# Kernel optimization log

Hardware: AMD Instinct MI355X
Metric: run time of the kernel (lower is better)

## Reference

```python
import jax, jax.numpy as jnp
import numpy as np

N = 100000   # nodes
E = 1250000  # directed edges
F = 32       # node_features
H = 64       # hidden_channels
C = 10       # num_classes
NEG_SLOPE = 0.2  # GATConv default LeakyReLU slope


def _glorot(key, shape):
    fan_in = shape[0]
    return jax.random.normal(key, shape, jnp.float32) / np.sqrt(fan_in)


def setup_inputs() -> dict:
    k = jax.random.split(jax.random.key(0), 16)
    x = jax.random.normal(k[0], (N, F), jnp.float32)
    edge_index = jax.random.randint(k[1], (2, E), 0, N, dtype=jnp.int32)
    return {
        "x": x,
        "edge_index": edge_index,
        # GCNConv 1
        "W1": _glorot(k[2], (F, H)), "b1": jnp.zeros((H,), jnp.float32),
        # GATConv (heads=1)
        "W2": _glorot(k[3], (H, H)),
        "a_src": _glorot(k[4], (H,)), "a_dst": _glorot(k[5], (H,)),
        "b2": jnp.zeros((H,), jnp.float32),
        # GCNConv 3
        "W3": _glorot(k[6], (H, H)), "b3": jnp.zeros((H,), jnp.float32),
        # optimization head
        "Wopt": _glorot(k[7], (H, C)), "bopt": jnp.zeros((C,), jnp.float32),
        # bottleneck detector MLP
        "Wb1": _glorot(k[8], (H, 32)), "bb1": jnp.zeros((32,), jnp.float32),
        "Wb2": _glorot(k[9], (32, 1)), "bb2": jnp.zeros((1,), jnp.float32),
    }


def _gcn_conv(x, W, b, src, dst, n):
    # PyG GCNConv: self-loops already appended to src/dst by caller.
    h = x @ W  # [n, out]
    deg = jnp.zeros((n,), x.dtype).at[dst].add(1.0)
    dinv = jax.lax.rsqrt(jnp.maximum(deg, 1e-12))
    norm = dinv[src] * dinv[dst]  # [e]
    msg = h[src] * norm[:, None]  # gather + scale
    out = jnp.zeros_like(h).at[dst].add(msg)  # scatter-add
    return out + b


def _gat_conv(x, W, a_src, a_dst, b, src, dst, n):
    # PyG GATConv, heads=1: self-loops already appended.
    h = x @ W  # [n, out]
    alpha_s = h @ a_src  # [n]
    alpha_d = h @ a_dst  # [n]
    e = jax.nn.leaky_relu(alpha_s[src] + alpha_d[dst], NEG_SLOPE)  # [e]
    # softmax over incoming edges of each dst node
    emax = jax.ops.segment_max(e, dst, num_segments=n)
    p = jnp.exp(e - emax[dst])
    denom = jax.ops.segment_sum(p, dst, num_segments=n)
    alpha = p / denom[dst]
    out = jnp.zeros_like(h).at[dst].add(h[src] * alpha[:, None])
    return out + b


def reference(x, edge_index, W1, b1, W2, a_src, a_dst, b2, W3, b3,
              Wopt, bopt, Wb1, bb1, Wb2, bb2):
    n = x.shape[0]
    loops = jnp.arange(n, dtype=edge_index.dtype)
    src = jnp.concatenate([edge_index[0], loops])
    dst = jnp.concatenate([edge_index[1], loops])

    h = jax.nn.relu(_gcn_conv(x, W1, b1, src, dst, n))
    h = jax.nn.relu(_gat_conv(h, W2, a_src, a_dst, b2, src, dst, n))
    h = jax.nn.relu(_gcn_conv(h, W3, b3, src, dst, n))

    optimizations = h @ Wopt + bopt                     # [n, C]
    bottlenecks = jax.nn.sigmoid(jax.nn.relu(h @ Wb1 + bb1) @ Wb2 + bb2)  # [n, 1]
    graph_embedding = h.mean(axis=0)                    # [H]
    return optimizations, bottlenecks, graph_embedding
```

## Files before the change

### kernel.cpp

```cpp
#include <hip/hip_runtime.h>
#include <hip/hip_bf16.h>


#define CAP 64
#define NP2 128
#define NB2MAX 800

__device__ __forceinline__ int uwave(){
  return __builtin_amdgcn_readfirstlane(threadIdx.x >> 6);
}
__device__ __forceinline__ unsigned short f2bf(float f){
  unsigned u = __float_as_uint(f);
  return (unsigned short)((u + 0x7fffu + ((u >> 16) & 1u)) >> 16);
}
__device__ __forceinline__ float bfl(unsigned u){ return __uint_as_float(u << 16); }
__device__ __forceinline__ float bfh(unsigned u){ return __uint_as_float(u & 0xffff0000u); }
__device__ __forceinline__ float rdlane(float v, int l){
  return __uint_as_float(__builtin_amdgcn_readlane(__float_as_uint(v), l));
}

__global__ void k_setup(const float* __restrict__ Wopt, const float* __restrict__ bopt,
                        const float* __restrict__ Wb1, const float* __restrict__ bb1,
                        float* __restrict__ Wcat, float* __restrict__ bcat,
                        int* __restrict__ bcnt, int* __restrict__ ghist,
                        unsigned short* __restrict__ tb,
                        unsigned short* __restrict__ xh, float* __restrict__ emb_acc,
                        float* __restrict__ als, int n, int nb2){
  int i = blockIdx.x*blockDim.x + threadIdx.x;
  if (i < nb2) bcnt[i] = 0;
  int tid = threadIdx.x;
  if (blockIdx.x == 1 && tid < 65) ghist[tid] = 0;
  if (blockIdx.x == 0){
    for (int j = tid; j < 4096; j += 256){
      int f = j >> 6, c = j & 63;
      float w = 0.f;
      if (c < 10)       w = Wopt[f*10 + c];
      else if (c >= 32) w = Wb1[f*32 + (c-32)];
      Wcat[j] = w;
    }
    if (tid < 64){
      float b = 0.f;
      if (tid < 10)       b = bopt[tid];
      else if (tid >= 32) b = bb1[tid-32];
      bcat[tid] = b;
      tb[(size_t)n*64 + tid] = 0;
      emb_acc[tid] = 0.f;
      if (tid == 0) als[n] = 0.f;
    }
    if (tid >= 64 && tid < 96) xh[(size_t)n*32 + (tid-64)] = 0;
  }
}

__global__ __launch_bounds__(256) void k_part(const int* __restrict__ src,
                        const int* __restrict__ dst,
                        uint2* __restrict__ pairs, int* __restrict__ bcnt,
                        int e, int nb2, int pbcap){
  __shared__ int lcnt[NB2MAX];
  __shared__ int lbase[NB2MAX];
  int tid = threadIdx.x;
  for (int j = tid; j < nb2; j += 256) lcnt[j] = 0;
  __syncthreads();
  int i0 = blockIdx.x*2048 + tid*8;
  int d[8], s[8], bk[8], lp[8];
  int nv = e - i0;
  if (nv > 8) nv = 8;
  if (nv < 0) nv = 0;
  if (nv == 8){
    int4 d0 = *(const int4*)(dst + i0), d1 = *(const int4*)(dst + i0 + 4);
    int4 s0 = *(const int4*)(src + i0), s1 = *(const int4*)(src + i0 + 4);
    d[0]=d0.x; d[1]=d0.y; d[2]=d0.z; d[3]=d0.w;
    d[4]=d1.x; d[5]=d1.y; d[6]=d1.z; d[7]=d1.w;
    s[0]=s0.x; s[1]=s0.y; s[2]=s0.z; s[3]=s0.w;
    s[4]=s1.x; s[5]=s1.y; s[6]=s1.z; s[7]=s1.w;
  } else {
    #pragma unroll
    for (int j = 0; j < 8; j++){ d[j] = 0; s[j] = 0; }
    for (int j = 0; j < nv; j++){ d[j] = dst[i0+j]; s[j] = src[i0+j]; }
  }
  #pragma unroll
  for (int j = 0; j < 8; j++){
    if (j < nv){
      bk[j] = d[j] >> 7;
      lp[j] = atomicAdd(&lcnt[bk[j]], 1);
    }
  }
  __syncthreads();
  for (int j = tid; j < nb2; j += 256){
    int c = lcnt[j];
    if (c) lbase[j] = atomicAdd(&bcnt[j], c);
  }
  __syncthreads();
  #pragma unroll
  for (int j = 0; j < 8; j++){
    if (j < nv){
      int p = lbase[bk[j]] + lp[j];
      if (p < pbcap)
        pairs[(size_t)bk[j]*pbcap + p] = make_uint2((unsigned)d[j], (unsigned)s[j]);
    }
  }
}

__global__ __launch_bounds__(256) void k_fill(const uint2* __restrict__ pairs,
                        const int* __restrict__ bcnt, int* __restrict__ cnt,
                        int* __restrict__ adj, int* __restrict__ ghist,
                        const float* __restrict__ x, unsigned short* __restrict__ xh,
                        int pbcap, int n){
  __shared__ int lc[NP2];
  __shared__ int ladj[NP2*CAP];
  __shared__ int lh[65];
  int b = blockIdx.x;
  int lo = b << 7;
  int nn = min(NP2, n - lo);
  int tid = threadIdx.x;
  for (int j = tid; j < NP2; j += 256) lc[j] = 0;
  if (tid < 65) lh[tid] = 0;
  int4 nfill = make_int4(n, n, n, n);
  for (int j = tid; j < NP2*CAP/4; j += 256) ((int4*)ladj)[j] = nfill;
  __syncthreads();
  int m = bcnt[b];
  if (m > pbcap) m = pbcap;
  const uint2* pb = pairs + (size_t)b*pbcap;
  for (int j = tid; j < m; j += 256){
    uint2 p = pb[j];
    int r = (int)p.x - lo;
    int pos = atomicAdd(&lc[r], 1);
    if (pos < CAP) ladj[(r << 6) + pos] = (int)p.y;
  }
  __syncthreads();
  if (tid < nn){
    int c = lc[tid];
    cnt[lo + tid] = c;
    atomicAdd(&lh[min(c, CAP)], 1);
  }
  __syncthreads();
  if (tid < 65 && lh[tid]) atomicAdd(&ghist[tid], lh[tid]);
  int tot = nn << 4;
  uint4* ga = (uint4*)(adj + (size_t)lo*CAP);
  const uint4* la = (const uint4*)ladj;
  for (int j = tid; j < tot; j += 256) ga[j] = la[j];
  int tf = nn << 3;
  const float4* xr4 = (const float4*)(x + (size_t)lo*32);
  uint2* xo = (uint2*)(xh + (size_t)lo*32);
  for (int j = tid; j < tf; j += 256){
    int r = j >> 3;
    float dv = rsqrtf((float)(lc[r] + 1));
    float4 v = xr4[j];
    uint2 o;
    o.x = (unsigned)f2bf(v.x*dv) | ((unsigned)f2bf(v.y*dv) << 16);
    o.y = (unsigned)f2bf(v.z*dv) | ((unsigned)f2bf(v.w*dv) << 16);
    xo[j] = o;
  }
}

__global__ void k_scan(const int* __restrict__ ghist, int* __restrict__ dbase){
  if (threadIdx.x == 0){
    int s = 0;
    for (int d = 0; d < 65; d++){ dbase[d] = s; s += ghist[d]; }
  }
}

__global__ __launch_bounds__(256) void k_perm(const int* __restrict__ cnt,
                        int* __restrict__ dbase, int* __restrict__ perm, int n){
  __shared__ int lh[65];
  __shared__ int lb[65];
  int tid = threadIdx.x;
  int v = blockIdx.x*256 + tid;
  if (tid < 65) lh[tid] = 0;
  __syncthreads();
  int d = 0, lp = 0;
  bool ok = v < n;
  if (ok){ d = min(cnt[v], CAP); lp = atomicAdd(&lh[d], 1); }
  __syncthreads();
  if (tid < 65 && lh[tid]) lb[tid] = atomicAdd(&dbase[tid], lh[tid]);
  __syncthreads();
  if (ok) perm[lb[d] + lp] = v;
}

__global__ __launch_bounds__(256) void k_agg32g(const unsigned short* __restrict__ xh,
                          const int* __restrict__ adj, const int* __restrict__ cnt,
                          const int* __restrict__ perm,
                          const float* __restrict__ W1, const float* __restrict__ b1,
                          unsigned short* __restrict__ h, int n){
  int lane = threadIdx.x & 63;
  float wreg[32];
  #pragma unroll
  for (int k = 0; k < 32; k++) wreg[k] = W1[k*64 + lane];
  float br = b1[lane];
  int i0 = blockIdx.x*8 + uwave()*2;
  if (i0 >= n) return;
  int i1 = i0 + 1;
  bool has1 = i1 < n;
  int v0 = perm[i0];
  int v1 = perm[has1 ? i1 : i0];
  int cn0 = cnt[v0], cn1 = cnt[v1];
  int c0 = min(cn0, CAP), c1 = min(cn1, CAP);
  int ureg0 = n, ureg1 = n;
  if (lane < c0) ureg0 = (adj + (size_t)v0*CAP)[lane];
  if (lane < c1) ureg1 = (adj + (size_t)v1*CAP)[lane];
  int g = lane >> 3, q = lane & 7;
  float4 a0 = {0.f,0.f,0.f,0.f}, a1 = {0.f,0.f,0.f,0.f};
  int itm = (max(c0, c1) + 7) >> 3;
  #pragma unroll 2
  for (int jj = 0; jj < itm; jj++){
    int u0 = __shfl(ureg0, jj*8 + g);
    int u1 = __shfl(ureg1, jj*8 + g);
    uint2 r0 = ((const uint2*)(xh + (size_t)u0*32))[q];
    uint2 r1 = ((const uint2*)(xh + (size_t)u1*32))[q];
    a0.x += bfl(r0.x); a0.y += bfh(r0.x); a0.z += bfl(r0.y); a0.w += bfh(r0.y);
    a1.x += bfl(r1.x); a1.y += bfh(r1.x); a1.z += bfl(r1.y); a1.w += bfh(r1.y);
  }
  #pragma unroll
  for (int off = 8; off <= 32; off <<= 1){
    a0.x += __shfl_xor(a0.x, off); a0.y += __shfl_xor(a0.y, off);
    a0.z += __shfl_xor(a0.z, off); a0.w += __shfl_xor(a0.w, off);
    a1.x += __shfl_xor(a1.x, off); a1.y += __shfl_xor(a1.y, off);
    a1.z += __shfl_xor(a1.z, off); a1.w += __shfl_xor(a1.w, off);
  }
  uint2 s0 = ((const uint2*)(xh + (size_t)v0*32))[q];
  uint2 s1 = ((const uint2*)(xh + (size_t)v1*32))[q];
  a0.x += bfl(s0.x); a0.y += bfh(s0.x); a0.z += bfl(s0.y); a0.w += bfh(s0.y);
  a1.x += bfl(s1.x); a1.y += bfh(s1.x); a1.z += bfl(s1.y); a1.w += bfh(s1.y);
  float dv0 = rsqrtf((float)(cn0 + 1)), dv1 = rsqrtf((float)(cn1 + 1));
  a0.x *= dv0; a0.y *= dv0; a0.z *= dv0; a0.w *= dv0;
  a1.x *= dv1; a1.y *= dv1; a1.z *= dv1; a1.w *= dv1;
  float h0 = br, h1v = br;
  #pragma unroll
  for (int q2 = 0; q2 < 8; q2++){
    float w0x = rdlane(a0.x, q2), w1x = rdlane(a1.x, q2);
    float w0y = rdlane(a0.y, q2), w1y = rdlane(a1.y, q2);
    float w0z = rdlane(a0.z, q2), w1z = rdlane(a1.z, q2);
    float w0w = rdlane(a0.w, q2), w1w = rdlane(a1.w, q2);
    h0 = fmaf(w0x, wreg[q2*4+0], h0); h1v = fmaf(w1x, wreg[q2*4+0], h1v);
    h0 = fmaf(w0y, wreg[q2*4+1], h0); h1v = fmaf(w1y, wreg[q2*4+1], h1v);
    h0 = fmaf(w0z, wreg[q2*4+2], h0); h1v = fmaf(w1z, wreg[q2*4+2], h1v);
    h0 = fmaf(w0w, wreg[q2*4+3], h0); h1v = fmaf(w1w, wreg[q2*4+3], h1v);
  }
  h[(size_t)v0*64 + lane] = f2bf(fmaxf(h0, 0.f));
  if (has1) h[(size_t)v1*64 + lane] = f2bf(fmaxf(h1v, 0.f));
}

template<bool SCALE>
__global__ __launch_bounds__(256, 4) void k_gemm_b(const unsigned short* __restrict__ x,
                       const float* __restrict__ W, const int* __restrict__ cnt,
                       unsigned short* __restrict__ t, int n){
  int lane = threadIdx.x & 63;
  int gw = blockIdx.x*4 + uwave();
  int nw = gridDim.x*4;
  float wreg[64];
  #pragma unroll
  for (int k = 0; k < 64; k++) wreg[k] = W[k*64 + lane];
  for (int v = gw; v < n; v += nw){
    const uint4* xr = (const uint4*)(x + (size_t)v*64);
    float acc = 0.f;
    #pragma unroll
    for (int k8 = 0; k8 < 8; k8++){
      uint4 c = xr[k8];
      acc = fmaf(bfl(c.x), wreg[k8*8+0], acc);
      acc = fmaf(bfh(c.x), wreg[k8*8+1], acc);
      acc = fmaf(bfl(c.y), wreg[k8*8+2], acc);
      acc = fmaf(bfh(c.y), wreg[k8*8+3], acc);
      acc = fmaf(bfl(c.z), wreg[k8*8+4], acc);
      acc = fmaf(bfh(c.z), wreg[k8*8+5], acc);
      acc = fmaf(bfl(c.w), wreg[k8*8+6], acc);
      acc = fmaf(bfh(c.w), wreg[k8*8+7], acc);
    }
    if (SCALE) acc *= rsqrtf((float)(cnt[v] + 1));
    t[(size_t)v*64 + lane] = f2bf(acc);
  }
}

__global__ __launch_bounds__(256, 4) void k_gemm_alpha(const unsigned short* __restrict__ x,
                       const float* __restrict__ W,
                       const float* __restrict__ asrc, const float* __restrict__ adst,
                       unsigned short* __restrict__ t, float* __restrict__ als,
                       float* __restrict__ ald, int n){
  int lane = threadIdx.x & 63;
  int gw = blockIdx.x*4 + uwave();
  int nw = gridDim.x*4;
  float wreg[64];
  #pragma unroll
  for (int k = 0; k < 64; k++) wreg[k] = W[k*64 + lane];
  float asr = asrc[lane], adr = adst[lane];
  for (int v = gw; v < n; v += nw){
    const uint4* xr = (const uint4*)(x + (size_t)v*64);
    float acc = 0.f;
    #pragma unroll
    for (int k8 = 0; k8 < 8; k8++){
      uint4 c = xr[k8];
      acc = fmaf(bfl(c.x), wreg[k8*8+0], acc);
      acc = fmaf(bfh(c.x), wreg[k8*8+1], acc);
      acc = fmaf(bfl(c.y), wreg[k8*8+2], acc);
      acc = fmaf(bfh(c.y), wreg[k8*8+3], acc);
      acc = fmaf(bfl(c.z), wreg[k8*8+4], acc);
      acc = fmaf(bfh(c.z), wreg[k8*8+5], acc);
      acc = fmaf(bfl(c.w), wreg[k8*8+6], acc);
      acc = fmaf(bfh(c.w), wreg[k8*8+7], acc);
    }
    t[(size_t)v*64 + lane] = f2bf(acc);
    float s1 = acc * asr, s2 = acc * adr;
    #pragma unroll
    for (int off = 32; off; off >>= 1){
      s1 += __shfl_xor(s1, off);
      s2 += __shfl_xor(s2, off);
    }
    if (lane == 0){ als[v] = s1; ald[v] = s2; }
  }
}

__global__ __launch_bounds__(256) void k_gcn_agg(const unsigned short* __restrict__ t,
                          const int* __restrict__ adj, const int* __restrict__ cnt,
                          const int* __restrict__ perm,
                          const float* __restrict__ b, unsigned short* __restrict__ h, int n){
  int lane = threadIdx.x & 63;
  int g = lane >> 3, q = lane & 7;
  int i0 = blockIdx.x*32 + uwave()*8;
  if (i0 >= n) return;
  int idx = i0 + g;
  bool vok = idx < n;
  int vg = perm[vok ? idx : n - 1];
  int cn = cnt[vg];
  int c = vok ? min(cn, CAP) : 0;
  int cm = c;
  cm = max(cm, __shfl_xor(cm, 8));
  cm = max(cm, __shfl_xor(cm, 16));
  cm = max(cm, __shfl_xor(cm, 32));
  int cmax = __builtin_amdgcn_readfirstlane(cm);
  const int* arow = adj + (size_t)vg*CAP;
  float a[8] = {0,0,0,0,0,0,0,0};
  int bsel = (lane & 56);
  for (int blk = 0; blk*8 < cmax; blk++){
    int ureg = arow[blk*8 + q];
    #pragma unroll
    for (int j2 = 0; j2 < 8; j2++){
      if (blk*8 + j2 >= cmax) break;
      int u = __shfl(ureg, bsel | j2);
      uint4 r = ((const uint4*)(t + (size_t)u*64))[q];
      a[0] += bfl(r.x); a[1] += bfh(r.x); a[2] += bfl(r.y); a[3] += bfh(r.y);
      a[4] += bfl(r.z); a[5] += bfh(r.z); a[6] += bfl(r.w); a[7] += bfh(r.w);
    }
  }
  uint4 s = ((const uint4*)(t + (size_t)vg*64))[q];
  a[0] += bfl(s.x); a[1] += bfh(s.x); a[2] += bfl(s.y); a[3] += bfh(s.y);
  a[4] += bfl(s.z); a[5] += bfh(s.z); a[6] += bfl(s.w); a[7] += bfh(s.w);
  float dv = rsqrtf((float)(cn + 1));
  float4 b0 = ((const float4*)b)[2*q], b1v = ((const float4*)b)[2*q+1];
  float r0 = fmaxf(fmaf(a[0], dv, b0.x), 0.f),  r1 = fmaxf(fmaf(a[1], dv, b0.y), 0.f);
  float r2 = fmaxf(fmaf(a[2], dv, b0.z), 0.f),  r3 = fmaxf(fmaf(a[3], dv, b0.w), 0.f);
  float r4 = fmaxf(fmaf(a[4], dv, b1v.x), 0.f), r5 = fmaxf(fmaf(a[5], dv, b1v.y), 0.f);
  float r6 = fmaxf(fmaf(a[6], dv, b1v.z), 0.f), r7 = fmaxf(fmaf(a[7], dv, b1v.w), 0.f);
  uint4 o;
  o.x = (unsigned)f2bf(r0) | ((unsigned)f2bf(r1) << 16);
  o.y = (unsigned)f2bf(r2) | ((unsigned)f2bf(r3) << 16);
  o.z = (unsigned)f2bf(r4) | ((unsigned)f2bf(r5) << 16);
  o.w = (unsigned)f2bf(r6) | ((unsigned)f2bf(r7) << 16);
  if (vok) ((uint4*)(h + (size_t)vg*64))[q] = o;
}

__global__ __launch_bounds__(256) void k_gat_agg(const unsigned short* __restrict__ t,
                          const int* __restrict__ adj, const int* __restrict__ cnt,
                          const int* __restrict__ perm,
                          const float* __restrict__ als, const float* __restrict__ ald,
                          const float* __restrict__ b, unsigned short* __restrict__ h, int n){
  int lane = threadIdx.x & 63;
  int g = lane >> 3, q = lane & 7;
  int i0 = blockIdx.x*32 + uwave()*8;
  if (i0 >= n) return;
  int idx = i0 + g;
  bool vok = idx < n;
  int vg = perm[vok ? idx : n - 1];
  int c = vok ? min(cnt[vg], CAP) : 0;
  int cm = c;
  cm = max(cm, __shfl_xor(cm, 8));
  cm = max(cm, __shfl_xor(cm, 16));
  cm = max(cm, __shfl_xor(cm, 32));
  int cmax = __builtin_amdgcn_readfirstlane(cm);
  const int* arow = adj + (size_t)vg*CAP;
  float adv = ald[vg];
  float es = als[vg] + adv; es = es > 0.f ? es : 0.2f*es;
  float er[8];
  float em = es;
  #pragma unroll
  for (int r = 0; r < 8; r++){
    if (r*8 >= cmax) break;
    int slot = r*8 + q;
    int u = arow[slot];
    float ev = als[u] + adv; ev = ev > 0.f ? ev : 0.2f*ev;
    er[r] = (slot < c) ? ev : -1e30f;
    em = fmaxf(em, er[r]);
  }
  em = fmaxf(em, __shfl_xor(em, 1));
  em = fmaxf(em, __shfl_xor(em, 2));
  em = fmaxf(em, __shfl_xor(em, 4));
  float sm = 0.f;
  #pragma unroll
  for (int r = 0; r < 8; r++){
    if (r*8 >= cmax) break;
    sm += ((r*8 + q) < c) ? __expf(er[r] - em) : 0.f;
  }
  sm += __shfl_xor(sm, 1);
  sm += __shfl_xor(sm, 2);
  sm += __shfl_xor(sm, 4);
  float ps = __expf(es - em);
  float inv = 1.f / (sm + ps);
  float a[8] = {0,0,0,0,0,0,0,0};
  int bsel = (lane & 56);
  for (int blk = 0; blk*8 < cmax; blk++){
    int ureg = arow[blk*8 + q];
    #pragma unroll
    for (int j2 = 0; j2 < 8; j2++){
      if (blk*8 + j2 >= cmax) break;
      int u = __shfl(ureg, bsel | j2);
      float ev = als[u] + adv; ev = ev > 0.f ? ev : 0.2f*ev;
      float w = __expf(ev - em);
      uint4 r = ((const uint4*)(t + (size_t)u*64))[q];
      a[0] = fmaf(w, bfl(r.x), a[0]); a[1] = fmaf(w, bfh(r.x), a[1]);
      a[2] = fmaf(w, bfl(r.y), a[2]); a[3] = fmaf(w, bfh(r.y), a[3]);
      a[4] = fmaf(w, bfl(r.z), a[4]); a[5] = fmaf(w, bfh(r.z), a[5]);
      a[6] = fmaf(w, bfl(r.w), a[6]); a[7] = fmaf(w, bfh(r.w), a[7]);
    }
  }
  uint4 s = ((const uint4*)(t + (size_t)vg*64))[q];
  a[0] = fmaf(ps, bfl(s.x), a[0]); a[1] = fmaf(ps, bfh(s.x), a[1]);
  a[2] = fmaf(ps, bfl(s.y), a[2]); a[3] = fmaf(ps, bfh(s.y), a[3]);
  a[4] = fmaf(ps, bfl(s.z), a[4]); a[5] = fmaf(ps, bfh(s.z), a[5]);
  a[6] = fmaf(ps, bfl(s.w), a[6]); a[7] = fmaf(ps, bfh(s.w), a[7]);
  float4 b0 = ((const float4*)b)[2*q], b1v = ((const float4*)b)[2*q+1];
  float r0 = fmaxf(fmaf(a[0], inv, b0.x), 0.f),  r1 = fmaxf(fmaf(a[1], inv, b0.y), 0.f);
  float r2 = fmaxf(fmaf(a[2], inv, b0.z), 0.f),  r3 = fmaxf(fmaf(a[3], inv, b0.w), 0.f);
  float r4 = fmaxf(fmaf(a[4], inv, b1v.x), 0.f), r5 = fmaxf(fmaf(a[5], inv, b1v.y), 0.f);
  float r6 = fmaxf(fmaf(a[6], inv, b1v.z), 0.f), r7 = fmaxf(fmaf(a[7], inv, b1v.w), 0.f);
  uint4 o;
  o.x = (unsigned)f2bf(r0) | ((unsigned)f2bf(r1) << 16);
  o.y = (unsigned)f2bf(r2) | ((unsigned)f2bf(r3) << 16);
  o.z = (unsigned)f2bf(r4) | ((unsigned)f2bf(r5) << 16);
  o.w = (unsigned)f2bf(r6) | ((unsigned)f2bf(r7) << 16);
  if (vok) ((uint4*)(h + (size_t)vg*64))[q] = o;
}

__global__ __launch_bounds__(256, 4) void k_heads(const unsigned short* __restrict__ h,
                        const float* __restrict__ Wcat, const float* __restrict__ bcat,
                        const float* __restrict__ Wb2, const float* __restrict__ bb2,
                        float* __restrict__ out_opt, float* __restrict__ out_bot, int n){
  int lane = threadIdx.x & 63;
  int gw = blockIdx.x*4 + uwave();
  int nw = gridDim.x*4;
  float wreg[64];
  #pragma unroll
  for (int k = 0; k < 64; k++) wreg[k] = Wcat[k*64 + lane];
  float bcr  = bcat[lane];
  float wb2r = (lane >= 32) ? Wb2[lane-32] : 0.f;
  float bb2r = bb2[0];
  for (int v = gw; v < n; v += nw){
    const uint4* xr = (const uint4*)(h + (size_t)v*64);
    float acc = bcr;
    #pragma unroll
    for (int k8 = 0; k8 < 8; k8++){
      uint4 c = xr[k8];
      acc = fmaf(bfl(c.x), wreg[k8*8+0], acc);
      acc = fmaf(bfh(c.x), wreg[k8*8+1], acc);
      acc = fmaf(bfl(c.y), wreg[k8*8+2], acc);
      acc = fmaf(bfh(c.y), wreg[k8*8+3], acc);
      acc = fmaf(bfl(c.z), wreg[k8*8+4], acc);
      acc = fmaf(bfh(c.z), wreg[k8*8+5], acc);
      acc = fmaf(bfl(c.w), wreg[k8*8+6], acc);
      acc = fmaf(bfh(c.w), wreg[k8*8+7], acc);
    }
    if (lane < 10) out_opt[(size_t)v*10 + lane] = acc;
    float contrib = fmaxf(acc, 0.f) * wb2r;
    #pragma unroll
    for (int off = 32; off; off >>= 1) contrib += __shfl_xor(contrib, off);
    if (lane == 0) out_bot[v] = 1.f / (1.f + __expf(-(contrib + bb2r)));
  }
}

__global__ __launch_bounds__(256) void k_mean(const unsigned short* __restrict__ h,
                       float* __restrict__ emb_acc, int n){
  __shared__ float red[256];
  int tid = threadIdx.x;
  int w = tid >> 6, lane = tid & 63;
  float s = 0.f;
  for (int r = blockIdx.x*4 + w; r < n; r += 1024)
    s += __uint_as_float(((unsigned)h[(size_t)r*64 + lane]) << 16);
  red[tid] = s;
  __syncthreads();
  if (tid < 64)
    atomicAdd(&emb_acc[tid], red[tid] + red[64+tid] + red[128+tid] + red[192+tid]);
}

__global__ void k_embed(const float* __restrict__ emb_acc, float* __restrict__ out_emb,
                        float invn){
  if (threadIdx.x < 64) out_emb[threadIdx.x] = emb_acc[threadIdx.x] * invn;
}

extern "C" void kernel_launch(void* const* d_in, const int* in_sizes, int n_in,
                              void* d_out, int out_size, void* d_ws, size_t ws_size,
                              hipStream_t stream) {
  const float* x    = (const float*)d_in[0];
  const int*   ei   = (const int*)d_in[1];
  const float* W1   = (const float*)d_in[2];
  const float* b1   = (const float*)d_in[3];
  const float* W2   = (const float*)d_in[4];
  const float* a_s  = (const float*)d_in[5];
  const float* a_d  = (const float*)d_in[6];
  const float* b2   = (const float*)d_in[7];
  const float* W3   = (const float*)d_in[8];
  const float* b3   = (const float*)d_in[9];
  const float* Wopt = (const float*)d_in[10];
  const float* bopt = (const float*)d_in[11];
  const float* Wb1  = (const float*)d_in[12];
  const float* bb1  = (const float*)d_in[13];
  const float* Wb2  = (const float*)d_in[14];
  const float* bb2  = (const float*)d_in[15];

  int n = in_sizes[0] / 32;
  int e = in_sizes[1] / 2;
  const int* src = ei;
  const int* dst = ei + e;

  char* ws = (char*)d_ws;
  size_t off = 0;
  auto alloc = [&](size_t bytes) -> void* {
    void* p = ws + off;
    off += (bytes + 255) & ~(size_t)255;
    return p;
  };
  int nb2 = (n + NP2 - 1) >> 7;
  int*            cnt     = (int*)           alloc((size_t)n * 4);
  int*            adj     = (int*)           alloc((size_t)n * CAP * 4);
  float*          als     = (float*)         alloc((size_t)(n+1) * 4);
  float*          ald     = (float*)         alloc((size_t)n * 4);
  unsigned short* xh      = (unsigned short*)alloc((size_t)(n+1) * 32 * 2);
  unsigned short* tb      = (unsigned short*)alloc((size_t)(n+1) * 64 * 2);
  unsigned short* hbuf    = (unsigned short*)alloc((size_t)n * 64 * 2);
  float*          emb_acc = (float*)         alloc((size_t)64 * 4);
  float*          Wcat    = (float*)         alloc((size_t)4096 * 4);
  float*          bcat    = (float*)         alloc((size_t)64 * 4);
  int*            bcnt    = (int*)           alloc((size_t)nb2 * 4);
  int*            ghist   = (int*)           alloc((size_t)65 * 4);
  int*            dbase   = (int*)           alloc((size_t)65 * 4);
  int*            perm    = (int*)           alloc((size_t)n * 4);

  int pbcap = e / nb2 + 384;
  long pcap_max = ((long)n * 128) / ((long)nb2 * 8);
  if (pbcap > (int)pcap_max) pbcap = (int)pcap_max;
  uint2* pairs = (uint2*)hbuf;

  float* out_opt = (float*)d_out;
  float* out_bot = out_opt + (size_t)n * 10;
  float* out_emb = out_bot + n;

  int nb8    = (n + 7) / 8;
  int nbW    = (n + 31) / 32;
  int nbN    = (n + 255) / 256;
  int nbP    = (e + 2047) / 2048;

  k_setup<<<nbN, 256, 0, stream>>>(Wopt, bopt, Wb1, bb1, Wcat, bcat,
                                   bcnt, ghist, tb, xh, emb_acc, als, n, nb2);
  k_part<<<nbP, 256, 0, stream>>>(src, dst, pairs, bcnt, e, nb2, pbcap);
  k_fill<<<nb2, 256, 0, stream>>>(pairs, bcnt, cnt, adj, ghist, x, xh, pbcap, n);
  k_scan<<<1, 64, 0, stream>>>(ghist, dbase);
  k_perm<<<nbN, 256, 0, stream>>>(cnt, dbase, perm, n);

  k_agg32g<<<nb8, 256, 0, stream>>>(xh, adj, cnt, perm, W1, b1, hbuf, n);

  k_gemm_alpha<<<1024, 256, 0, stream>>>(hbuf, W2, a_s, a_d, tb, als, ald, n);
  k_gat_agg<<<nbW, 256, 0, stream>>>(tb, adj, cnt, perm, als, ald, b2, hbuf, n);

  k_gemm_b<true><<<1024, 256, 0, stream>>>(hbuf, W3, cnt, tb, n);
  k_gcn_agg<<<nbW, 256, 0, stream>>>(tb, adj, cnt, perm, b3, hbuf, n);

  k_heads<<<1024, 256, 0, stream>>>(hbuf, Wcat, bcat, Wb2, bb2,
                                    out_opt, out_bot, n);
  k_mean<<<256, 256, 0, stream>>>(hbuf, emb_acc, n);
  k_embed<<<1, 64, 0, stream>>>(emb_acc, out_emb, 1.0f / (float)n);
}
```

Baseline: 357.6 us.

## Replace global degree-sorted permutation with per-block local degree sort in fill

```diff
diff --git a/kernel.cpp b/kernel.cpp
--- a/kernel.cpp
+++ b/kernel.cpp
@@ -22,15 +22,13 @@
 __global__ void k_setup(const float* __restrict__ Wopt, const float* __restrict__ bopt,
                         const float* __restrict__ Wb1, const float* __restrict__ bb1,
                         float* __restrict__ Wcat, float* __restrict__ bcat,
-                        int* __restrict__ bcnt, int* __restrict__ ghist,
-                        unsigned short* __restrict__ tb,
+                        int* __restrict__ bcnt, unsigned short* __restrict__ tb,
                         unsigned short* __restrict__ xh, float* __restrict__ emb_acc,
                         float* __restrict__ als, int n, int nb2){
   int i = blockIdx.x*blockDim.x + threadIdx.x;
   if (i < nb2) bcnt[i] = 0;
-  int tid = threadIdx.x;
-  if (blockIdx.x == 1 && tid < 65) ghist[tid] = 0;
   if (blockIdx.x == 0){
+    int tid = threadIdx.x;
     for (int j = tid; j < 4096; j += 256){
       int f = j >> 6, c = j & 63;
       float w = 0.f;
@@ -102,18 +100,18 @@
 
 __global__ __launch_bounds__(256) void k_fill(const uint2* __restrict__ pairs,
                         const int* __restrict__ bcnt, int* __restrict__ cnt,
-                        int* __restrict__ adj, int* __restrict__ ghist,
+                        int* __restrict__ adj, int* __restrict__ perm,
                         const float* __restrict__ x, unsigned short* __restrict__ xh,
                         int pbcap, int n){
   __shared__ int lc[NP2];
   __shared__ int ladj[NP2*CAP];
-  __shared__ int lh[65];
+  __shared__ int lb[65];
   int b = blockIdx.x;
   int lo = b << 7;
   int nn = min(NP2, n - lo);
   int tid = threadIdx.x;
   for (int j = tid; j < NP2; j += 256) lc[j] = 0;
-  if (tid < 65) lh[tid] = 0;
+  if (tid < 65) lb[tid] = 0;
   int4 nfill = make_int4(n, n, n, n);
   for (int j = tid; j < NP2*CAP/4; j += 256) ((int4*)ladj)[j] = nfill;
   __syncthreads();
@@ -127,13 +125,24 @@
     if (pos < CAP) ladj[(r << 6) + pos] = (int)p.y;
   }
   __syncthreads();
+  int d = 0;
   if (tid < nn){
     int c = lc[tid];
     cnt[lo + tid] = c;
-    atomicAdd(&lh[min(c, CAP)], 1);
-  }
-  __syncthreads();
-  if (tid < 65 && lh[tid]) atomicAdd(&ghist[tid], lh[tid]);
+    d = min(c, CAP);
+    atomicAdd(&lb[d], 1);
+  }
+  __syncthreads();
+  if (tid == 0){
+    int s = 0;
+    #pragma unroll 1
+    for (int k = 0; k < 65; k++){ int c = lb[k]; lb[k] = s; s += c; }
+  }
+  __syncthreads();
+  if (tid < nn){
+    int p = atomicAdd(&lb[d], 1);
+    perm[lo + p] = lo + tid;
+  }
   int tot = nn << 4;
   uint4* ga = (uint4*)(adj + (size_t)lo*CAP);
   const uint4* la = (const uint4*)ladj;
@@ -150,30 +159,6 @@
     o.y = (unsigned)f2bf(v.z*dv) | ((unsigned)f2bf(v.w*dv) << 16);
     xo[j] = o;
   }
-}
-
-__global__ void k_scan(const int* __restrict__ ghist, int* __restrict__ dbase){
-  if (threadIdx.x == 0){
-    int s = 0;
-    for (int d = 0; d < 65; d++){ dbase[d] = s; s += ghist[d]; }
-  }
-}
-
-__global__ __launch_bounds__(256) void k_perm(const int* __restrict__ cnt,
-                        int* __restrict__ dbase, int* __restrict__ perm, int n){
-  __shared__ int lh[65];
-  __shared__ int lb[65];
-  int tid = threadIdx.x;
-  int v = blockIdx.x*256 + tid;
-  if (tid < 65) lh[tid] = 0;
-  __syncthreads();
-  int d = 0, lp = 0;
-  bool ok = v < n;
-  if (ok){ d = min(cnt[v], CAP); lp = atomicAdd(&lh[d], 1); }
-  __syncthreads();
-  if (tid < 65 && lh[tid]) lb[tid] = atomicAdd(&dbase[tid], lh[tid]);
-  __syncthreads();
-  if (ok) perm[lb[d] + lp] = v;
 }
 
 __global__ __launch_bounds__(256) void k_agg32g(const unsigned short* __restrict__ xh,
@@ -536,8 +521,6 @@
   float*          Wcat    = (float*)         alloc((size_t)4096 * 4);
   float*          bcat    = (float*)         alloc((size_t)64 * 4);
   int*            bcnt    = (int*)           alloc((size_t)nb2 * 4);
-  int*            ghist   = (int*)           alloc((size_t)65 * 4);
-  int*            dbase   = (int*)           alloc((size_t)65 * 4);
   int*            perm    = (int*)           alloc((size_t)n * 4);
 
   int pbcap = e / nb2 + 384;
@@ -555,11 +538,9 @@
   int nbP    = (e + 2047) / 2048;
 
   k_setup<<<nbN, 256, 0, stream>>>(Wopt, bopt, Wb1, bb1, Wcat, bcat,
-                                   bcnt, ghist, tb, xh, emb_acc, als, n, nb2);
+                                   bcnt, tb, xh, emb_acc, als, n, nb2);
   k_part<<<nbP, 256, 0, stream>>>(src, dst, pairs, bcnt, e, nb2, pbcap);
-  k_fill<<<nb2, 256, 0, stream>>>(pairs, bcnt, cnt, adj, ghist, x, xh, pbcap, n);
-  k_scan<<<1, 64, 0, stream>>>(ghist, dbase);
-  k_perm<<<nbN, 256, 0, stream>>>(cnt, dbase, perm, n);
+  k_fill<<<nb2, 256, 0, stream>>>(pairs, bcnt, cnt, adj, perm, x, xh, pbcap, n);
 
   k_agg32g<<<nb8, 256, 0, stream>>>(xh, adj, cnt, perm, W1, b1, hbuf, n);
 
```

New measurement: 353.2 us. Within noise of the previous version (-1.3%).
